# Kernel tuning notes

Hardware: AMD Instinct MI355X
Metric: run time of the kernel (lower is better)

The kernel has to match this reference:

```python
import jax, jax.numpy as jnp
import numpy as np

B, S, D, H = 2, 2048, 1024, 16
DK = D // H

def setup_inputs() -> dict:
    key = jax.random.key(0)
    ks = jax.random.split(key, 7)
    query = jax.random.normal(ks[0], (B, S, D), dtype=jnp.float32)
    k_in = jax.random.normal(ks[1], (B, S, D), dtype=jnp.float32)
    v_in = jax.random.normal(ks[2], (B, S, D), dtype=jnp.float32)
    mask = jnp.ones((B, 1, 1, S), dtype=jnp.int32)
    # Xavier-uniform weights for square Linear layers (bias=False)
    limit = np.sqrt(6.0 / (D + D)).astype(np.float32)
    def w(k):
        return jax.random.uniform(k, (D, D), dtype=jnp.float32, minval=-limit, maxval=limit)
    return {"query": query, "key": k_in, "value": v_in, "mask": mask,
            "Wq": w(ks[3]), "Wk": w(ks[4]), "Wv": w(ks[5]), "Wo": w(ks[6])}

def reference(query, key, value, mask, Wq, Wk, Wv, Wo):
    b, sq, _ = query.shape
    # torch Linear: x @ W.T
    Q = (query @ Wq.T).reshape(b, sq, H, DK).transpose(0, 2, 1, 3)   # [B,H,Sq,DK]
    K = (key   @ Wk.T).reshape(b, -1, H, DK).transpose(0, 2, 1, 3)   # [B,H,Sk,DK]
    V = (value @ Wv.T).reshape(b, -1, H, DK).transpose(0, 2, 1, 3)   # [B,H,Sk,DK]
    scores = jnp.einsum("bhqd,bhkd->bhqk", Q, K) / jnp.sqrt(jnp.float32(DK))
    scores = jnp.where(mask == 0, jnp.float32(-1e9), scores)
    attn = jax.nn.softmax(scores, axis=-1)                            # [B,H,Sq,Sk]
    out = jnp.einsum("bhqk,bhkd->bhqd", attn, V)                      # [B,H,Sq,DK]
    out = out.transpose(0, 2, 1, 3).reshape(b, sq, D)
    output = out @ Wo.T
    return output, attn
```

## Files before the change

kernel.cpp:

```cpp
#include <hip/hip_runtime.h>
#include <hip/hip_bf16.h>
#include <stdint.h>

using s16x8 = __attribute__((ext_vector_type(8))) short;
using f32x4 = __attribute__((ext_vector_type(4))) float;
typedef __hip_bfloat16 bf16;

static constexpr int NS = 2048, ND = 1024;
static constexpr size_t OUT0E = (size_t)4096 * 1024;

__device__ __forceinline__ void gload_lds16(const void* g, void* l) {
  __builtin_amdgcn_global_load_lds((const __attribute__((address_space(1))) uint32_t*)g,
                                   (__attribute__((address_space(3))) uint32_t*)l, 16, 0, 0);
}
__device__ __forceinline__ float b2f(uint16_t v) {
  union { uint32_t u; float f; } c; c.u = ((uint32_t)v) << 16; return c.f;
}

__global__ __launch_bounds__(256) void cvt3_kernel(
    const float* __restrict__ s0, const float* __restrict__ s1,
    const float* __restrict__ s2, bf16* __restrict__ d0,
    bf16* __restrict__ d1, bf16* __restrict__ d2, int n8) {
  const int z = blockIdx.z;
  const float* src = (z == 0) ? s0 : (z == 1) ? s1 : s2;
  bf16* dst = (z == 0) ? d0 : (z == 1) ? d1 : d2;
  const int i = blockIdx.x * 256 + threadIdx.x;
  if (i >= n8) return;
  const float4 a = ((const float4*)src)[2 * i];
  const float4 b = ((const float4*)src)[2 * i + 1];
  bf16 t[8];
  t[0] = __float2bfloat16(a.x); t[1] = __float2bfloat16(a.y);
  t[2] = __float2bfloat16(a.z); t[3] = __float2bfloat16(a.w);
  t[4] = __float2bfloat16(b.x); t[5] = __float2bfloat16(b.y);
  t[6] = __float2bfloat16(b.z); t[7] = __float2bfloat16(b.w);
  *(s16x8*)(dst + 8 * (size_t)i) = *(const s16x8*)t;
}

__global__ __launch_bounds__(256) void cvt_kernel(const float* __restrict__ src,
                                                  bf16* __restrict__ dst, int n8) {
  const int i = blockIdx.x * 256 + threadIdx.x;
  if (i >= n8) return;
  const float4 a = ((const float4*)src)[2 * i];
  const float4 b = ((const float4*)src)[2 * i + 1];
  bf16 t[8];
  t[0] = __float2bfloat16(a.x); t[1] = __float2bfloat16(a.y);
  t[2] = __float2bfloat16(a.z); t[3] = __float2bfloat16(a.w);
  t[4] = __float2bfloat16(b.x); t[5] = __float2bfloat16(b.y);
  t[6] = __float2bfloat16(b.z); t[7] = __float2bfloat16(b.w);
  *(s16x8*)(dst + 8 * (size_t)i) = *(const s16x8*)t;
}

__device__ __forceinline__ void gemm128(const bf16* __restrict__ A, const bf16* __restrict__ W,
                                        int m0, int n0, char* AsmB, char* BsmB,
                                        f32x4 acc[4][4]) {
  const int tid = threadIdx.x;
  const int w = tid >> 6, lane = tid & 63;
  const int r16 = lane & 15, g = lane >> 4;
  const int wr = (w >> 1) * 64, wc = (w & 1) * 64;
  const int o0 = tid * 16, o1 = o0 + 4096;
  const char* Ab = (const char*)A;
  const char* Wb = (const char*)W;
  const size_t rA0 = (size_t)(m0 + (o0 >> 6)) * 2048 + (o0 & 63);
  const size_t rA1 = (size_t)(m0 + (o1 >> 6)) * 2048 + (o1 & 63);
  const size_t rW0 = (size_t)(n0 + (o0 >> 6)) * 2048 + (o0 & 63);
  const size_t rW1 = (size_t)(n0 + (o1 >> 6)) * 2048 + (o1 & 63);
  for (int kt = 0; kt < 32; ++kt) {
    const size_t kb = (size_t)kt * 64;
    gload_lds16(Ab + rA0 + kb, AsmB + w * 1024);
    gload_lds16(Ab + rA1 + kb, AsmB + 4096 + w * 1024);
    gload_lds16(Wb + rW0 + kb, BsmB + w * 1024);
    gload_lds16(Wb + rW1 + kb, BsmB + 4096 + w * 1024);
    __syncthreads();
    s16x8 af[4], bfr[4];
#pragma unroll
    for (int m = 0; m < 4; ++m)
      af[m] = *(const s16x8*)(AsmB + (wr + m * 16 + r16) * 64 + g * 16);
#pragma unroll
    for (int n = 0; n < 4; ++n)
      bfr[n] = *(const s16x8*)(BsmB + (wc + n * 16 + r16) * 64 + g * 16);
#pragma unroll
    for (int m = 0; m < 4; ++m)
#pragma unroll
      for (int n = 0; n < 4; ++n)
        acc[m][n] = __builtin_amdgcn_mfma_f32_16x16x32_bf16(af[m], bfr[n], acc[m][n], 0, 0, 0);
    __syncthreads();
  }
}

__global__ __launch_bounds__(256) void qkv_proj_kernel(
    const bf16* __restrict__ xq, const bf16* __restrict__ xk, const bf16* __restrict__ xv,
    const bf16* __restrict__ wq, const bf16* __restrict__ wk, const bf16* __restrict__ wv,
    bf16* __restrict__ q_b, bf16* __restrict__ k_b, bf16* __restrict__ vt) {
  __shared__ __align__(16) char Asm[8192];
  __shared__ __align__(16) char Bsm[8192];
  const int z = blockIdx.z;
  const bf16* A = (z == 0) ? xq : (z == 1) ? xk : xv;
  const bf16* W = (z == 0) ? wq : (z == 1) ? wk : wv;
  const int m0 = blockIdx.y * 128, n0 = blockIdx.x * 128;
  f32x4 acc[4][4] = {};
  gemm128(A, W, m0, n0, Asm, Bsm, acc);
  const int tid = threadIdx.x, w = tid >> 6, lane = tid & 63;
  const int r16 = lane & 15, g = lane >> 4;
  const int wr = (w >> 1) * 64, wc = (w & 1) * 64;
#pragma unroll
  for (int m = 0; m < 4; ++m)
#pragma unroll
    for (int n = 0; n < 4; ++n)
#pragma unroll
      for (int j = 0; j < 4; ++j) {
        const int gr = m0 + wr + m * 16 + g * 4 + j;
        const int gc = n0 + wc + n * 16 + r16;
        const int b = gr >> 11, s = gr & 2047;
        const bf16 val = __float2bfloat16(acc[m][n][j]);
        if (z == 2) {
          vt[((size_t)b * 1024 + gc) * 2048 + s] = val;
        } else {
          bf16* dst = (z == 0) ? q_b : k_b;
          dst[(((size_t)(b * 16 + (gc >> 6))) * 2048 + s) * 64 + (gc & 63)] = val;
        }
      }
}

__global__ __launch_bounds__(256) void oproj_kernel(
    const bf16* __restrict__ ao, const bf16* __restrict__ wo, float* __restrict__ out) {
  __shared__ __align__(16) char Asm[8192];
  __shared__ __align__(16) char Bsm[8192];
  const int m0 = blockIdx.y * 128, n0 = blockIdx.x * 128;
  f32x4 acc[4][4] = {};
  gemm128(ao, wo, m0, n0, Asm, Bsm, acc);
  const int tid = threadIdx.x, w = tid >> 6, lane = tid & 63;
  const int r16 = lane & 15, g = lane >> 4;
  const int wr = (w >> 1) * 64, wc = (w & 1) * 64;
#pragma unroll
  for (int m = 0; m < 4; ++m)
#pragma unroll
    for (int n = 0; n < 4; ++n)
#pragma unroll
      for (int j = 0; j < 4; ++j) {
        const int gr = m0 + wr + m * 16 + g * 4 + j;
        const int gc = n0 + wc + n * 16 + r16;
        out[(size_t)gr * 1024 + gc] = acc[m][n][j];
      }
}

__device__ __forceinline__ void attn_remap(int flat, int& bh, int& q0) {
  const int xcd = flat & 7, idx = flat >> 3;
  bh = xcd * 4 + (idx >> 5);
  q0 = (idx & 31) * 64;
}

__global__ __launch_bounds__(256) void attn_rsum_kernel(
    const bf16* __restrict__ q_b, const bf16* __restrict__ k_b,
    float* __restrict__ rinv_out) {
  __shared__ __align__(16) char Ksm[16384];
  __shared__ float rs_lds[4][64];

  const int tid = threadIdx.x, w = tid >> 6, lane = tid & 63;
  const int r16 = lane & 15, g = lane >> 4;
  int bh, q0;
  attn_remap(blockIdx.x, bh, q0);

  const bf16* Qh = q_b + (size_t)bh * (NS * 64);
  const char* Kh = (const char*)(k_b + (size_t)bh * (NS * 64));

  s16x8 qf[4][2];
#pragma unroll
  for (int m = 0; m < 4; ++m)
#pragma unroll
    for (int ks = 0; ks < 2; ++ks)
      qf[m][ks] = *(const s16x8*)(Qh + (size_t)(q0 + m * 16 + r16) * 64 + ks * 32 + g * 8);

  float rsum[4][4];
#pragma unroll
  for (int m = 0; m < 4; ++m)
#pragma unroll
    for (int j = 0; j < 4; ++j) rsum[m][j] = 0.f;

  for (int kt = 0; kt < 16; ++kt) {
#pragma unroll
    for (int r = 0; r < 4; ++r) {
      const int o = r * 4096 + tid * 16;
      const int sw = o ^ (((o >> 7) & 7) << 4);
      gload_lds16(Kh + (size_t)kt * 16384 + sw, Ksm + r * 4096 + w * 1024);
    }
    __syncthreads();

    f32x4 sc[4][2] = {};
#pragma unroll
    for (int ks = 0; ks < 2; ++ks) {
      s16x8 kf[2];
#pragma unroll
      for (int n = 0; n < 2; ++n) {
        const int kv = w * 32 + n * 16 + r16;
        const int t = kv * 128 + ks * 64 + g * 16;
        kf[n] = *(const s16x8*)(Ksm + (t ^ ((kv & 7) << 4)));
      }
#pragma unroll
      for (int m = 0; m < 4; ++m)
#pragma unroll
        for (int n = 0; n < 2; ++n)
          sc[m][n] = __builtin_amdgcn_mfma_f32_16x16x32_bf16(qf[m][ks], kf[n], sc[m][n], 0, 0, 0);
    }
#pragma unroll
    for (int m = 0; m < 4; ++m)
#pragma unroll
      for (int n = 0; n < 2; ++n)
#pragma unroll
        for (int j = 0; j < 4; ++j)
          rsum[m][j] += __expf(sc[m][n][j] * 0.125f);
    __syncthreads();
  }

#pragma unroll
  for (int m = 0; m < 4; ++m)
#pragma unroll
    for (int j = 0; j < 4; ++j) {
      float v = rsum[m][j];
      v += __shfl_xor(v, 1);
      v += __shfl_xor(v, 2);
      v += __shfl_xor(v, 4);
      v += __shfl_xor(v, 8);
      rsum[m][j] = v;
    }
  if (r16 == 0) {
#pragma unroll
    for (int m = 0; m < 4; ++m)
#pragma unroll
      for (int j = 0; j < 4; ++j) rs_lds[w][m * 16 + g * 4 + j] = rsum[m][j];
  }
  __syncthreads();
  if (tid < 64) {
    const float t = rs_lds[0][tid] + rs_lds[1][tid] + rs_lds[2][tid] + rs_lds[3][tid];
    rinv_out[(size_t)bh * NS + q0 + tid] = 1.0f / t;
  }
}

__global__ __launch_bounds__(256) void attn_write_kernel(
    const bf16* __restrict__ q_b, const bf16* __restrict__ k_b,
    const bf16* __restrict__ vt_, const float* __restrict__ rinv,
    float* __restrict__ attn_out, bf16* __restrict__ ao_ws) {
  __shared__ __align__(16) char Ksm[8192];
  __shared__ __align__(16) char Vsm[8192];
  __shared__ __align__(16) bf16 Psm[64 * 72];

  const int tid = threadIdx.x, w = tid >> 6, lane = tid & 63;
  const int r16 = lane & 15, g = lane >> 4;
  int bh, q0;
  attn_remap(blockIdx.x, bh, q0);
  const int b = bh >> 4, h = bh & 15;

  const bf16* Qh = q_b + (size_t)bh * (NS * 64);
  const char* Kh = (const char*)(k_b + (size_t)bh * (NS * 64));
  const char* Vh = (const char*)(vt_ + ((size_t)b * 1024 + h * 64) * 2048);
  float* attn_h = attn_out + (size_t)bh * ((size_t)NS * NS);

  s16x8 qf[4][2];
#pragma unroll
  for (int m = 0; m < 4; ++m)
#pragma unroll
    for (int ks = 0; ks < 2; ++ks)
      qf[m][ks] = *(const s16x8*)(Qh + (size_t)(q0 + m * 16 + r16) * 64 + ks * 32 + g * 8);

  float rv[4][4];
  {
    const float* rb = rinv + (size_t)bh * NS + q0;
#pragma unroll
    for (int m = 0; m < 4; ++m)
#pragma unroll
      for (int j = 0; j < 4; ++j) rv[m][j] = rb[m * 16 + g * 4 + j];
  }

  f32x4 oacc[4] = {};

  for (int kt = 0; kt < 32; ++kt) {
#pragma unroll
    for (int r = 0; r < 2; ++r) {
      const int o = r * 4096 + tid * 16;
      const int sw = o ^ (((o >> 7) & 7) << 4);
      gload_lds16(Kh + (size_t)kt * 8192 + sw, Ksm + r * 4096 + w * 1024);
      gload_lds16(Vh + (size_t)(o >> 7) * 4096 + (size_t)kt * 128 +
                      ((o & 127) ^ (((o >> 7) & 7) << 4)),
                  Vsm + r * 4096 + w * 1024);
    }
    __syncthreads();

    f32x4 sc[4] = {};
#pragma unroll
    for (int ks = 0; ks < 2; ++ks) {
      const int kv = w * 16 + r16;
      const int t = kv * 128 + ks * 64 + g * 16;
      const s16x8 kf = *(const s16x8*)(Ksm + (t ^ ((kv & 7) << 4)));
#pragma unroll
      for (int m = 0; m < 4; ++m)
        sc[m] = __builtin_amdgcn_mfma_f32_16x16x32_bf16(qf[m][ks], kf, sc[m], 0, 0, 0);
    }

#pragma unroll
    for (int m = 0; m < 4; ++m)
#pragma unroll
      for (int j = 0; j < 4; ++j) {
        const int row = m * 16 + g * 4 + j;
        const int col = w * 16 + r16;
        const float p = __expf(sc[m][j] * 0.125f) * rv[m][j];
        Psm[row * 72 + col] = __float2bfloat16(p);
      }
    __syncthreads();

#pragma unroll
    for (int i = 0; i < 4; ++i) {
      const int f = i * 256 + tid;
      const int row = f >> 4, c4 = f & 15;
      const uint16_t* ps = (const uint16_t*)((const char*)Psm + row * 144 + c4 * 8);
      float4 v;
      v.x = b2f(ps[0]); v.y = b2f(ps[1]); v.z = b2f(ps[2]); v.w = b2f(ps[3]);
      *(float4*)(attn_h + (size_t)(q0 + row) * 2048 + kt * 64 + c4 * 4) = v;
    }

#pragma unroll
    for (int ks2 = 0; ks2 < 2; ++ks2) {
      s16x8 pf[4], vfr;
#pragma unroll
      for (int m = 0; m < 4; ++m)
        pf[m] = *(const s16x8*)((const char*)Psm + (m * 16 + r16) * 144 + ks2 * 64 + g * 16);
      {
        const int dk = w * 16 + r16;
        const int t = dk * 128 + ks2 * 64 + g * 16;
        vfr = *(const s16x8*)(Vsm + (t ^ ((dk & 7) << 4)));
      }
#pragma unroll
      for (int m = 0; m < 4; ++m)
        oacc[m] = __builtin_amdgcn_mfma_f32_16x16x32_bf16(pf[m], vfr, oacc[m], 0, 0, 0);
    }
    __syncthreads();
  }

#pragma unroll
  for (int m = 0; m < 4; ++m)
#pragma unroll
    for (int j = 0; j < 4; ++j) {
      const int s = q0 + m * 16 + g * 4 + j;
      ao_ws[((size_t)b * NS + s) * 1024 + h * 64 + w * 16 + r16] =
          __float2bfloat16(oacc[m][j]);
    }
}

extern "C" void kernel_launch(void* const* d_in, const int* in_sizes, int n_in,
                              void* d_out, int out_size, void* d_ws, size_t ws_size,
                              hipStream_t stream) {
  const float* q_f  = (const float*)d_in[0];
  const float* k_f  = (const float*)d_in[1];
  const float* v_f  = (const float*)d_in[2];
  const float* wq_f = (const float*)d_in[4];
  const float* wk_f = (const float*)d_in[5];
  const float* wv_f = (const float*)d_in[6];
  const float* wo_f = (const float*)d_in[7];

  float* out0  = (float*)d_out;
  float* attnf = out0 + OUT0E;
  const size_t MB = 1u << 20;

  char* as = (char*)attnf;
  bf16* xq_b = (bf16*)(as);
  bf16* xk_b = (bf16*)(as + 8 * MB);
  bf16* xv_b = (bf16*)(as + 16 * MB);
  bf16* wq_b = (bf16*)(as + 24 * MB);
  bf16* wk_b = (bf16*)(as + 26 * MB);
  bf16* wv_b = (bf16*)(as + 28 * MB);

  char* ws = (char*)d_ws;
  bf16*  q_b   = (bf16*)(ws);
  bf16*  k_b   = (bf16*)(ws + 8 * MB);
  bf16*  vt    = (bf16*)(ws + 16 * MB);
  bf16*  ao    = (bf16*)(ws + 24 * MB);
  float* rinvb = (float*)(ws + 32 * MB);
  bf16*  wo_b  = (bf16*)(ws + 16 * MB);

  dim3 blk(256);
  const int nx8 = 4096 * 1024 / 8;
  const int nw8 = 1024 * 1024 / 8;
  cvt3_kernel<<<dim3(nx8 / 256, 1, 3), blk, 0, stream>>>(q_f, k_f, v_f,
                                                         xq_b, xk_b, xv_b, nx8);
  cvt3_kernel<<<dim3(nw8 / 256, 1, 3), blk, 0, stream>>>(wq_f, wk_f, wv_f,
                                                         wq_b, wk_b, wv_b, nw8);

  qkv_proj_kernel<<<dim3(8, 32, 3), blk, 0, stream>>>(xq_b, xk_b, xv_b,
                                                      wq_b, wk_b, wv_b,
                                                      q_b, k_b, vt);

  attn_rsum_kernel<<<dim3(1024), blk, 0, stream>>>(q_b, k_b, rinvb);
  attn_write_kernel<<<dim3(1024), blk, 0, stream>>>(q_b, k_b, vt, rinvb, attnf, ao);

  cvt_kernel<<<dim3(nw8 / 256), blk, 0, stream>>>(wo_f, wo_b, nw8);
  oproj_kernel<<<dim3(8, 32), blk, 0, stream>>>(ao, wo_b, out0);
}
```

Baseline: 321.5 us.

## Fuse attention row-sum and write kernels; retile output projection to 64-row blocks

Merges the softmax normalizer pass and the attention-write pass into one kernel. Row reciprocals now stay in LDS instead of going through a global buffer, and Q fragments are loaded once, which removes a launch and a global round trip. The output projection now uses 64x128 tiles, giving 512 blocks instead of 256 for better occupancy across CUs. The Wo conversion moves to the start of the stream, with its buffer relocated so it no longer aliases vt. The fused kernel uses more LDS per block, which may lower occupancy.

After: 313.9 us. 1.02x faster.

```diff
diff --git a/kernel.cpp b/kernel.cpp
--- a/kernel.cpp
+++ b/kernel.cpp
@@ -121,26 +121,44 @@
       }
 }
 
-__global__ __launch_bounds__(256) void oproj_kernel(
+__global__ __launch_bounds__(256) void oproj64_kernel(
     const bf16* __restrict__ ao, const bf16* __restrict__ wo, float* __restrict__ out) {
-  __shared__ __align__(16) char Asm[8192];
+  __shared__ __align__(16) char Asm[4096];
   __shared__ __align__(16) char Bsm[8192];
-  const int m0 = blockIdx.y * 128, n0 = blockIdx.x * 128;
-  f32x4 acc[4][4] = {};
-  gemm128(ao, wo, m0, n0, Asm, Bsm, acc);
   const int tid = threadIdx.x, w = tid >> 6, lane = tid & 63;
   const int r16 = lane & 15, g = lane >> 4;
-  const int wr = (w >> 1) * 64, wc = (w & 1) * 64;
-#pragma unroll
-  for (int m = 0; m < 4; ++m)
-#pragma unroll
-    for (int n = 0; n < 4; ++n)
-#pragma unroll
-      for (int j = 0; j < 4; ++j) {
-        const int gr = m0 + wr + m * 16 + g * 4 + j;
-        const int gc = n0 + wc + n * 16 + r16;
-        out[(size_t)gr * 1024 + gc] = acc[m][n][j];
-      }
+  const int m0 = blockIdx.y * 64, n0 = blockIdx.x * 128;
+  const int o0 = tid * 16, o1 = o0 + 4096;
+  const char* Ab = (const char*)ao;
+  const char* Wb = (const char*)wo;
+  const size_t rA  = (size_t)(m0 + (o0 >> 6)) * 2048 + (o0 & 63);
+  const size_t rB0 = (size_t)(n0 + (o0 >> 6)) * 2048 + (o0 & 63);
+  const size_t rB1 = (size_t)(n0 + (o1 >> 6)) * 2048 + (o1 & 63);
+  f32x4 acc[8] = {};
+  for (int kt = 0; kt < 32; ++kt) {
+    const size_t kb = (size_t)kt * 64;
+    gload_lds16(Ab + rA + kb, Asm + w * 1024);
+    gload_lds16(Wb + rB0 + kb, Bsm + w * 1024);
+    gload_lds16(Wb + rB1 + kb, Bsm + 4096 + w * 1024);
+    __syncthreads();
+    const s16x8 af = *(const s16x8*)(Asm + (w * 16 + r16) * 64 + g * 16);
+    s16x8 bfr[8];
+#pragma unroll
+    for (int n = 0; n < 8; ++n)
+      bfr[n] = *(const s16x8*)(Bsm + (n * 16 + r16) * 64 + g * 16);
+#pragma unroll
+    for (int n = 0; n < 8; ++n)
+      acc[n] = __builtin_amdgcn_mfma_f32_16x16x32_bf16(af, bfr[n], acc[n], 0, 0, 0);
+    __syncthreads();
+  }
+#pragma unroll
+  for (int n = 0; n < 8; ++n)
+#pragma unroll
+    for (int j = 0; j < 4; ++j) {
+      const int gr = m0 + w * 16 + g * 4 + j;
+      const int gc = n0 + n * 16 + r16;
+      out[(size_t)gr * 1024 + gc] = acc[n][j];
+    }
 }
 
 __device__ __forceinline__ void attn_remap(int flat, int& bh, int& q0) {
@@ -149,19 +167,24 @@
   q0 = (idx & 31) * 64;
 }
 
-__global__ __launch_bounds__(256) void attn_rsum_kernel(
+__global__ __launch_bounds__(256) void attn_fused_kernel(
     const bf16* __restrict__ q_b, const bf16* __restrict__ k_b,
-    float* __restrict__ rinv_out) {
-  __shared__ __align__(16) char Ksm[16384];
-  __shared__ float rs_lds[4][64];
+    const bf16* __restrict__ vt_, float* __restrict__ attn_out,
+    bf16* __restrict__ ao_ws) {
+  __shared__ __align__(16) char KV[25600];
+  __shared__ float red_lds[4][64];
+  __shared__ float rinv_lds[64];
 
   const int tid = threadIdx.x, w = tid >> 6, lane = tid & 63;
   const int r16 = lane & 15, g = lane >> 4;
   int bh, q0;
   attn_remap(blockIdx.x, bh, q0);
+  const int b = bh >> 4, h = bh & 15;
 
   const bf16* Qh = q_b + (size_t)bh * (NS * 64);
   const char* Kh = (const char*)(k_b + (size_t)bh * (NS * 64));
+  const char* Vh = (const char*)(vt_ + ((size_t)b * 1024 + h * 64) * 2048);
+  float* attn_h = attn_out + (size_t)bh * ((size_t)NS * NS);
 
   s16x8 qf[4][2];
 #pragma unroll
@@ -181,10 +204,9 @@
     for (int r = 0; r < 4; ++r) {
       const int o = r * 4096 + tid * 16;
       const int sw = o ^ (((o >> 7) & 7) << 4);
-      gload_lds16(Kh + (size_t)kt * 16384 + sw, Ksm + r * 4096 + w * 1024);
-    }
-    __syncthreads();
-
+      gload_lds16(Kh + (size_t)kt * 16384 + sw, KV + r * 4096 + w * 1024);
+    }
+    __syncthreads();
     f32x4 sc[4][2] = {};
 #pragma unroll
     for (int ks = 0; ks < 2; ++ks) {
@@ -193,7 +215,7 @@
       for (int n = 0; n < 2; ++n) {
         const int kv = w * 32 + n * 16 + r16;
         const int t = kv * 128 + ks * 64 + g * 16;
-        kf[n] = *(const s16x8*)(Ksm + (t ^ ((kv & 7) << 4)));
+        kf[n] = *(const s16x8*)(KV + (t ^ ((kv & 7) << 4)));
       }
 #pragma unroll
       for (int m = 0; m < 4; ++m)
@@ -226,52 +248,25 @@
 #pragma unroll
     for (int m = 0; m < 4; ++m)
 #pragma unroll
-      for (int j = 0; j < 4; ++j) rs_lds[w][m * 16 + g * 4 + j] = rsum[m][j];
+      for (int j = 0; j < 4; ++j) red_lds[w][m * 16 + g * 4 + j] = rsum[m][j];
   }
   __syncthreads();
   if (tid < 64) {
-    const float t = rs_lds[0][tid] + rs_lds[1][tid] + rs_lds[2][tid] + rs_lds[3][tid];
-    rinv_out[(size_t)bh * NS + q0 + tid] = 1.0f / t;
-  }
-}
-
-__global__ __launch_bounds__(256) void attn_write_kernel(
-    const bf16* __restrict__ q_b, const bf16* __restrict__ k_b,
-    const bf16* __restrict__ vt_, const float* __restrict__ rinv,
-    float* __restrict__ attn_out, bf16* __restrict__ ao_ws) {
-  __shared__ __align__(16) char Ksm[8192];
-  __shared__ __align__(16) char Vsm[8192];
-  __shared__ __align__(16) bf16 Psm[64 * 72];
-
-  const int tid = threadIdx.x, w = tid >> 6, lane = tid & 63;
-  const int r16 = lane & 15, g = lane >> 4;
-  int bh, q0;
-  attn_remap(blockIdx.x, bh, q0);
-  const int b = bh >> 4, h = bh & 15;
-
-  const bf16* Qh = q_b + (size_t)bh * (NS * 64);
-  const char* Kh = (const char*)(k_b + (size_t)bh * (NS * 64));
-  const char* Vh = (const char*)(vt_ + ((size_t)b * 1024 + h * 64) * 2048);
-  float* attn_h = attn_out + (size_t)bh * ((size_t)NS * NS);
-
-  s16x8 qf[4][2];
-#pragma unroll
-  for (int m = 0; m < 4; ++m)
-#pragma unroll
-    for (int ks = 0; ks < 2; ++ks)
-      qf[m][ks] = *(const s16x8*)(Qh + (size_t)(q0 + m * 16 + r16) * 64 + ks * 32 + g * 8);
-
+    const float t = red_lds[0][tid] + red_lds[1][tid] + red_lds[2][tid] + red_lds[3][tid];
+    rinv_lds[tid] = 1.0f / t;
+  }
+  __syncthreads();
   float rv[4][4];
-  {
-    const float* rb = rinv + (size_t)bh * NS + q0;
-#pragma unroll
-    for (int m = 0; m < 4; ++m)
-#pragma unroll
-      for (int j = 0; j < 4; ++j) rv[m][j] = rb[m * 16 + g * 4 + j];
-  }
+#pragma unroll
+  for (int m = 0; m < 4; ++m)
+#pragma unroll
+    for (int j = 0; j < 4; ++j) rv[m][j] = rinv_lds[m * 16 + g * 4 + j];
+
+  char* Ksm = KV;
+  char* Vsm = KV + 8192;
+  bf16* Psm = (bf16*)(KV + 16384);
 
   f32x4 oacc[4] = {};
-
   for (int kt = 0; kt < 32; ++kt) {
 #pragma unroll
     for (int r = 0; r < 2; ++r) {
@@ -368,16 +363,16 @@
   bf16* wv_b = (bf16*)(as + 28 * MB);
 
   char* ws = (char*)d_ws;
-  bf16*  q_b   = (bf16*)(ws);
-  bf16*  k_b   = (bf16*)(ws + 8 * MB);
-  bf16*  vt    = (bf16*)(ws + 16 * MB);
-  bf16*  ao    = (bf16*)(ws + 24 * MB);
-  float* rinvb = (float*)(ws + 32 * MB);
-  bf16*  wo_b  = (bf16*)(ws + 16 * MB);
+  bf16* q_b  = (bf16*)(ws);
+  bf16* k_b  = (bf16*)(ws + 8 * MB);
+  bf16* vt   = (bf16*)(ws + 16 * MB);
+  bf16* ao   = (bf16*)(ws + 24 * MB);
+  bf16* wo_b = (bf16*)(ws + 32 * MB);
 
   dim3 blk(256);
   const int nx8 = 4096 * 1024 / 8;
   const int nw8 = 1024 * 1024 / 8;
+  cvt_kernel<<<dim3(nw8 / 256), blk, 0, stream>>>(wo_f, wo_b, nw8);
   cvt3_kernel<<<dim3(nx8 / 256, 1, 3), blk, 0, stream>>>(q_f, k_f, v_f,
                                                          xq_b, xk_b, xv_b, nx8);
   cvt3_kernel<<<dim3(nw8 / 256, 1, 3), blk, 0, stream>>>(wq_f, wk_f, wv_f,
@@ -387,9 +382,7 @@
                                                       wq_b, wk_b, wv_b,
                                                       q_b, k_b, vt);
 
-  attn_rsum_kernel<<<dim3(1024), blk, 0, stream>>>(q_b, k_b, rinvb);
-  attn_write_kernel<<<dim3(1024), blk, 0, stream>>>(q_b, k_b, vt, rinvb, attnf, ao);
-
-  cvt_kernel<<<dim3(nw8 / 256), blk, 0, stream>>>(wo_f, wo_b, nw8);
-  oproj_kernel<<<dim3(8, 32), blk, 0, stream>>>(ao, wo_b, out0);
-}
+  attn_fused_kernel<<<dim3(1024), blk, 0, stream>>>(q_b, k_b, vt, attnf, ao);
+
+  oproj64_kernel<<<dim3(8, 64), blk, 0, stream>>>(ao, wo_b, out0);
+}
```
